# Performance work log

Hardware: AMD Instinct MI355X
Metric: run time of the kernel (lower is better)

## Reference

```python
import jax, jax.numpy as jnp
import numpy as np

N_HEAD, D_HEAD, D_MODEL = 8, 64, 512
QLEN, MLEN, BSZ = 1024, 1024, 4
KLEN = QLEN + MLEN
SCALE = 1.0 / (D_HEAD ** 0.5)
LN_EPS = 1e-5


def _rel_shift(x):
    # x: [qlen, rlen, bsz, n_head]
    q, rl, b, n = x.shape
    zero_pad = jnp.zeros((q, 1, b, n), x.dtype)
    x_padded = jnp.concatenate([zero_pad, x], axis=1).reshape(rl + 1, q, b, n)
    return x_padded[1:].reshape(q, rl, b, n)


def _layer_norm(x, g, b):
    mu = jnp.mean(x, axis=-1, keepdims=True)
    var = jnp.var(x, axis=-1, keepdims=True)
    return (x - mu) * jax.lax.rsqrt(var + LN_EPS) * g + b


def setup_inputs() -> dict:
    key = jax.random.key(0)
    ks = jax.random.split(key, 10)
    s = 0.02
    return {
        "w": jax.random.normal(ks[0], (QLEN, BSZ, D_MODEL), jnp.float32),
        "r": jax.random.normal(ks[1], (KLEN, 1, D_MODEL), jnp.float32),
        "r_w_bias": jax.random.normal(ks[2], (N_HEAD, D_HEAD), jnp.float32) * s,
        "r_r_bias": jax.random.normal(ks[3], (N_HEAD, D_HEAD), jnp.float32) * s,
        "mems": jax.random.normal(ks[4], (MLEN, BSZ, D_MODEL), jnp.float32),
        "Wq": jax.random.normal(ks[5], (D_MODEL, N_HEAD * D_HEAD), jnp.float32) * s,
        "Wkv": jax.random.normal(ks[6], (D_MODEL, 2 * N_HEAD * D_HEAD), jnp.float32) * s,
        "Wr": jax.random.normal(ks[7], (D_MODEL, N_HEAD * D_HEAD), jnp.float32) * s,
        "Wo": jax.random.normal(ks[8], (N_HEAD * D_HEAD, D_MODEL), jnp.float32) * s,
        "ln_g": jnp.ones((D_MODEL,), jnp.float32),
        "ln_b": jnp.zeros((D_MODEL,), jnp.float32),
        # causal mask: query i can attend keys j <= i + MLEN
        "attn_mask": jnp.arange(KLEN)[None, :] > (jnp.arange(QLEN) + MLEN)[:, None],
    }


def reference(w, r, r_w_bias, r_r_bias, mems, Wq, Wkv, Wr, Wo, ln_g, ln_b, attn_mask):
    qlen, bsz = w.shape[0], w.shape[1]
    cat = jnp.concatenate([mems, w], axis=0)          # [klen, bsz, d_model]
    klen = cat.shape[0]

    r_head_k = (r[:, 0] @ Wr).reshape(-1, N_HEAD, D_HEAD)   # [rlen, n, d]
    kv = cat @ Wkv                                           # [klen, bsz, 2*n*d]
    w_head_k, w_head_v = jnp.split(kv, 2, axis=-1)
    w_head_q = (cat[-qlen:] @ Wq).reshape(qlen, bsz, N_HEAD, D_HEAD)
    w_head_k = w_head_k.reshape(klen, bsz, N_HEAD, D_HEAD)
    w_head_v = w_head_v.reshape(klen, bsz, N_HEAD, D_HEAD)

    AC = jnp.einsum('ibnd,jbnd->ijbn', w_head_q + r_w_bias, w_head_k)
    BD = jnp.einsum('ibnd,jnd->ijbn', w_head_q + r_r_bias, r_head_k)
    BD = _rel_shift(BD)[:, :klen]

    attn_score = (AC + BD) * SCALE                           # [qlen, klen, bsz, n]
    attn_score = jnp.where(attn_mask[:, :, None, None], -jnp.inf, attn_score)
    attn_prob = jax.nn.softmax(attn_score, axis=1)

    attn_vec = jnp.einsum('ijbn,jbnd->ibnd', attn_prob, w_head_v)
    attn_vec = attn_vec.reshape(qlen, bsz, N_HEAD * D_HEAD)
    attn_out = attn_vec @ Wo
    return _layer_norm(w + attn_out, ln_g, ln_b)
```

## Files before the change

kernel.cpp:

```cpp
#include <hip/hip_runtime.h>
#include <hip/hip_bf16.h>
#include <math.h>

#define QLEN 1024
#define MLEN 1024
#define KLEN 2048
#define BSZ 4
#define NH 8
#define DH 64
#define DM 512
#define SCALE 0.125f
#define LN_EPS 1e-5f

#define RK_ROWS 2112
#define DSTR 95

typedef __attribute__((ext_vector_type(8))) short short8;
typedef __attribute__((ext_vector_type(4))) float float4_;

#define GLB(p) ((const __attribute__((address_space(1))) void*)(p))
#define LDSP(p) ((__attribute__((address_space(3))) void*)(p))

__device__ inline ushort to_bf16(float x) {
  __hip_bfloat16 h = __float2bfloat16(x);
  return *reinterpret_cast<ushort*>(&h);
}
__device__ inline float bf16_to_f(ushort u) {
  union { unsigned int i; float f; } v;
  v.i = (unsigned int)u << 16;
  return v.f;
}

__device__ inline float row_max16(float v) {
  int x = __builtin_bit_cast(int, v);
  v = fmaxf(v, __builtin_bit_cast(float, __builtin_amdgcn_update_dpp(x, x, 0xB1, 0xF, 0xF, false)));
  x = __builtin_bit_cast(int, v);
  v = fmaxf(v, __builtin_bit_cast(float, __builtin_amdgcn_update_dpp(x, x, 0x4E, 0xF, 0xF, false)));
  x = __builtin_bit_cast(int, v);
  v = fmaxf(v, __builtin_bit_cast(float, __builtin_amdgcn_update_dpp(x, x, 0x124, 0xF, 0xF, false)));
  x = __builtin_bit_cast(int, v);
  v = fmaxf(v, __builtin_bit_cast(float, __builtin_amdgcn_update_dpp(x, x, 0x128, 0xF, 0xF, false)));
  return v;
}
__device__ inline float row_sum16(float v) {
  int x = __builtin_bit_cast(int, v);
  v += __builtin_bit_cast(float, __builtin_amdgcn_update_dpp(x, x, 0xB1, 0xF, 0xF, false));
  x = __builtin_bit_cast(int, v);
  v += __builtin_bit_cast(float, __builtin_amdgcn_update_dpp(x, x, 0x4E, 0xF, 0xF, false));
  x = __builtin_bit_cast(int, v);
  v += __builtin_bit_cast(float, __builtin_amdgcn_update_dpp(x, x, 0x124, 0xF, 0xF, false));
  x = __builtin_bit_cast(int, v);
  v += __builtin_bit_cast(float, __builtin_amdgcn_update_dpp(x, x, 0x128, 0xF, 0xF, false));
  return v;
}

__global__ __launch_bounds__(256) void wtrans_all(
    const float* __restrict__ Wq, const float* __restrict__ Wkv,
    const float* __restrict__ Wr, const float* __restrict__ Wo,
    ushort* __restrict__ WqT, ushort* __restrict__ WkvT,
    ushort* __restrict__ WrT, ushort* __restrict__ WoT) {
  __shared__ ushort tile[32][33];
  const int z = blockIdx.z;
  const float* W;
  ushort* WT;
  int N;
  if (z == 0)      { W = Wq;  WT = WqT;  N = DM; }
  else if (z == 1) { W = Wkv; WT = WkvT; N = 2 * DM; }
  else if (z == 2) { W = Wr;  WT = WrT;  N = DM; }
  else             { W = Wo;  WT = WoT;  N = DM; }
  const int k0 = blockIdx.x * 32, n0 = blockIdx.y * 32;
  if (n0 >= N) return;
  const int tid = threadIdx.x;
#pragma unroll
  for (int it = 0; it < 4; ++it) {
    int idx = tid + it * 256;
    int r = idx >> 5, c = idx & 31;
    tile[r][c] = to_bf16(W[(size_t)(k0 + r) * N + n0 + c]);
  }
  __syncthreads();
#pragma unroll
  for (int it = 0; it < 4; ++it) {
    int idx = tid + it * 256;
    int r = idx >> 5, c = idx & 31;
    WT[(size_t)(n0 + r) * DM + k0 + c] = tile[c][r];
  }
}

__global__ __launch_bounds__(256) void proj_all(
    const float* __restrict__ w, const float* __restrict__ mems,
    const float* __restrict__ r,
    const ushort* __restrict__ WqT, const ushort* __restrict__ WkvT,
    const ushort* __restrict__ WrT,
    const float* __restrict__ bias0, const float* __restrict__ bias1,
    ushort* __restrict__ qw, ushort* __restrict__ qr,
    ushort* __restrict__ k2, ushort* __restrict__ v2,
    ushort* __restrict__ rk2) {
  __shared__ ushort As[128 * 32];
  __shared__ ushort Bs[128 * 32];
  const int tid = threadIdx.x;
  int mode, bx, by;
  {
    int id = blockIdx.x;
    if (id < 128)      { mode = 0; bx = id >> 2;         by = id & 3; }
    else if (id < 640) { mode = 1; bx = (id - 128) >> 3; by = (id - 128) & 7; }
    else               { mode = 2; bx = (id - 640) >> 2; by = (id - 640) & 3; }
  }
  const int m0 = bx * 128, n0 = by * 128;
  const int wv = tid >> 6, lane = tid & 63;
  const int wm = wv >> 1, wn = wv & 1;
  const int l16 = lane & 15, quad = lane >> 4;

  const int arow = tid >> 1;
  const int acol = (tid & 1) * 16;
  const float* asrc;
  {
    int m = m0 + arow;
    if (mode == 2) asrc = r + (size_t)m * DM;
    else asrc = (m < QLEN * BSZ) ? w + (size_t)m * DM
                                 : mems + (size_t)(m - QLEN * BSZ) * DM;
    asrc += acol;
  }
  const ushort* BT = (mode == 0) ? WqT : (mode == 1) ? WkvT : WrT;
  const ushort* bsrc = BT + (size_t)(n0 + arow) * DM + acol;

  float4_ acc[4][4];
#pragma unroll
  for (int a = 0; a < 4; ++a)
#pragma unroll
    for (int b = 0; b < 4; ++b) acc[a][b] = float4_{0.f, 0.f, 0.f, 0.f};

  for (int k0 = 0; k0 < DM; k0 += 32) {
    float4 a0 = *reinterpret_cast<const float4*>(asrc + k0);
    float4 a1 = *reinterpret_cast<const float4*>(asrc + k0 + 4);
    float4 a2 = *reinterpret_cast<const float4*>(asrc + k0 + 8);
    float4 a3 = *reinterpret_cast<const float4*>(asrc + k0 + 12);
    ushort4 u0, u1, u2, u3;
    u0.x = to_bf16(a0.x); u0.y = to_bf16(a0.y); u0.z = to_bf16(a0.z); u0.w = to_bf16(a0.w);
    u1.x = to_bf16(a1.x); u1.y = to_bf16(a1.y); u1.z = to_bf16(a1.z); u1.w = to_bf16(a1.w);
    u2.x = to_bf16(a2.x); u2.y = to_bf16(a2.y); u2.z = to_bf16(a2.z); u2.w = to_bf16(a2.w);
    u3.x = to_bf16(a3.x); u3.y = to_bf16(a3.y); u3.z = to_bf16(a3.z); u3.w = to_bf16(a3.w);
    *reinterpret_cast<ushort4*>(&As[arow * 32 + acol]) = u0;
    *reinterpret_cast<ushort4*>(&As[arow * 32 + acol + 4]) = u1;
    *reinterpret_cast<ushort4*>(&As[arow * 32 + acol + 8]) = u2;
    *reinterpret_cast<ushort4*>(&As[arow * 32 + acol + 12]) = u3;
    *reinterpret_cast<uint4*>(&Bs[arow * 32 + acol]) =
        *reinterpret_cast<const uint4*>(bsrc + k0);
    *reinterpret_cast<uint4*>(&Bs[arow * 32 + acol + 8]) =
        *reinterpret_cast<const uint4*>(bsrc + k0 + 8);
    __syncthreads();
    short8 af[4], bf[4];
#pragma unroll
    for (int f = 0; f < 4; ++f) {
      af[f] = *reinterpret_cast<const short8*>(&As[(wm * 64 + f * 16 + l16) * 32 + quad * 8]);
      bf[f] = *reinterpret_cast<const short8*>(&Bs[(wn * 64 + f * 16 + l16) * 32 + quad * 8]);
    }
#pragma unroll
    for (int fm = 0; fm < 4; ++fm)
#pragma unroll
      for (int fn = 0; fn < 4; ++fn)
        acc[fm][fn] = __builtin_amdgcn_mfma_f32_16x16x32_bf16(bf[fn], af[fm], acc[fm][fn], 0, 0, 0);
    __syncthreads();
  }

#pragma unroll
  for (int fm = 0; fm < 4; ++fm) {
#pragma unroll
    for (int fn = 0; fn < 4; ++fn) {
      const int mm = m0 + wm * 64 + fm * 16 + l16;
      const int nnb = n0 + wn * 64 + fn * 16 + quad * 4;
      const float4_ a = acc[fm][fn];
      if (mode == 0) {
        float4 b0v = *reinterpret_cast<const float4*>(bias0 + nnb);
        float4 b1v = *reinterpret_cast<const float4*>(bias1 + nnb);
        int i = mm >> 2, b = mm & 3;
        int hd = nnb >> 6, d0 = nnb & 63;
        size_t idx = (((size_t)(b * NH + hd)) * QLEN + i) * DH + d0;
        ushort4 o0, o1;
        o0.x = to_bf16(a[0] + b0v.x); o0.y = to_bf16(a[1] + b0v.y);
        o0.z = to_bf16(a[2] + b0v.z); o0.w = to_bf16(a[3] + b0v.w);
        o1.x = to_bf16(a[0] + b1v.x); o1.y = to_bf16(a[1] + b1v.y);
        o1.z = to_bf16(a[2] + b1v.z); o1.w = to_bf16(a[3] + b1v.w);
        *reinterpret_cast<ushort4*>(qw + idx) = o0;
        *reinterpret_cast<ushort4*>(qr + idx) = o1;
      } else if (mode == 1) {
        int pos = mm >> 2, b = mm & 3;
        int jb = pos >> 5, jj = pos & 31;
        if (nnb < DM) {
          int hd = nnb >> 6, d = nnb & 63;
          int bn = b * NH + hd;
          int tile = ((jj >> 4) << 1) | (d >> 5);
          int lane2 = (((d >> 3) & 3) << 4) | (jj & 15);
          ushort4 o;
          o.x = to_bf16(a[0]); o.y = to_bf16(a[1]);
          o.z = to_bf16(a[2]); o.w = to_bf16(a[3]);
          *reinterpret_cast<ushort4*>(
              k2 + ((((size_t)bn * 64 + jb) * 4 + tile) * 64 + lane2) * 8 + (d & 7)) = o;
        } else {
          int nn2 = nnb - DM;
          int hd = nn2 >> 6, d = nn2 & 63;
          int bn = b * NH + hd;
          int tile = d >> 4;
          size_t base = ((((size_t)bn * 64 + jb) * 4 + tile) * 64 +
                         ((jj >> 3) << 4)) * 8 + (jj & 7);
#pragma unroll
          for (int reg = 0; reg < 4; ++reg)
            v2[base + (size_t)((d & 15) + reg) * 8] = to_bf16(a[reg]);
        }
      } else {
        int t = mm;
        int hd = nnb >> 6, d = nnb & 63;
        ushort4 o;
        o.x = to_bf16(a[0]); o.y = to_bf16(a[1]);
        o.z = to_bf16(a[2]); o.w = to_bf16(a[3]);
        *reinterpret_cast<ushort4*>(
            rk2 + ((size_t)hd * RK_ROWS + t) * DH + d) = o;
      }
    }
  }
}

__device__ inline uint4 combine8(uint4 u0, uint4 u1, float s0, float s1) {
  union U { uint4 v; ushort u[8]; };
  U a, b, o;
  a.v = u0; b.v = u1;
#pragma unroll
  for (int e = 0; e < 8; ++e)
    o.u[e] = to_bf16(bf16_to_f(a.u[e]) * s0 + bf16_to_f(b.u[e]) * s1);
  return o.v;
}

__global__ __launch_bounds__(256) void mfma_out(
    const ushort* __restrict__ O0, const ushort* __restrict__ O1,
    const float* __restrict__ ml, const ushort* __restrict__ BT,
    float* __restrict__ Y) {
  __shared__ ushort As[128 * 32];
  __shared__ ushort Bs[128 * 32];
  const int tid = threadIdx.x;
  const int m0 = blockIdx.x * 128, n0 = blockIdx.y * 128;
  const int wv = tid >> 6, lane = tid & 63;
  const int wm = wv >> 1, wn = wv & 1;
  const int l16 = lane & 15, quad = lane >> 4;
  const int arow = tid >> 1;
  const int acol = (tid & 1) * 16;
  const int row = m0 + arow;
  const ushort* bsrc = BT + (size_t)(n0 + arow) * DM + acol;
  const float2* mlp = (const float2*)ml;

  float4_ acc[4][4];
#pragma unroll
  for (int a = 0; a < 4; ++a)
#pragma unroll
    for (int b = 0; b < 4; ++b) acc[a][b] = float4_{0.f, 0.f, 0.f, 0.f};

  for (int k0 = 0; k0 < DM; k0 += 32) {
    const int col0 = k0 + acol;
    const int h = col0 >> 6;
    float2 a = mlp[(size_t)row * NH + h];
    float2 c = mlp[(size_t)(QLEN * BSZ + row) * NH + h];
    float M = fmaxf(a.x, c.x);
    float e0 = __builtin_amdgcn_exp2f(a.x - M);
    float e1 = __builtin_amdgcn_exp2f(c.x - M);
    float inv = 1.f / (a.y * e0 + c.y * e1);
    float s0 = e0 * inv, s1 = e1 * inv;
    size_t ob = (size_t)row * DM + col0;
    uint4 u0a = *reinterpret_cast<const uint4*>(O0 + ob);
    uint4 u0b = *reinterpret_cast<const uint4*>(O0 + ob + 8);
    uint4 u1a = *reinterpret_cast<const uint4*>(O1 + ob);
    uint4 u1b = *reinterpret_cast<const uint4*>(O1 + ob + 8);
    *reinterpret_cast<uint4*>(&As[arow * 32 + acol]) = combine8(u0a, u1a, s0, s1);
    *reinterpret_cast<uint4*>(&As[arow * 32 + acol + 8]) = combine8(u0b, u1b, s0, s1);
    *reinterpret_cast<uint4*>(&Bs[arow * 32 + acol]) = *reinterpret_cast<const uint4*>(bsrc + k0);
    *reinterpret_cast<uint4*>(&Bs[arow * 32 + acol + 8]) = *reinterpret_cast<const uint4*>(bsrc + k0 + 8);
    __syncthreads();
    short8 af[4], bf[4];
#pragma unroll
    for (int f = 0; f < 4; ++f) {
      af[f] = *reinterpret_cast<const short8*>(&As[(wm * 64 + f * 16 + l16) * 32 + quad * 8]);
      bf[f] = *reinterpret_cast<const short8*>(&Bs[(wn * 64 + f * 16 + l16) * 32 + quad * 8]);
    }
#pragma unroll
    for (int fm = 0; fm < 4; ++fm)
#pragma unroll
      for (int fn = 0; fn < 4; ++fn)
        acc[fm][fn] = __builtin_amdgcn_mfma_f32_16x16x32_bf16(bf[fn], af[fm], acc[fm][fn], 0, 0, 0);
    __syncthreads();
  }
#pragma unroll
  for (int fm = 0; fm < 4; ++fm)
#pragma unroll
    for (int fn = 0; fn < 4; ++fn) {
      int mm = m0 + wm * 64 + fm * 16 + l16;
      int nnb = n0 + wn * 64 + fn * 16 + quad * 4;
      float4 o;
      o.x = acc[fm][fn][0]; o.y = acc[fm][fn][1];
      o.z = acc[fm][fn][2]; o.w = acc[fm][fn][3];
      *reinterpret_cast<float4*>(Y + (size_t)mm * DM + nnb) = o;
    }
}

__global__ __launch_bounds__(256) void ln_fuse(
    const float* __restrict__ y, const float* __restrict__ wres,
    const float* __restrict__ g, const float* __restrict__ bb,
    float* __restrict__ out) {
  const int row = blockIdx.x * 4 + (threadIdx.x >> 6);
  const int lane = threadIdx.x & 63;
  const float* yr = y + (size_t)row * DM + lane * 4;
  const float* wr = wres + (size_t)row * DM + lane * 4;
  float4 x0 = *(const float4*)yr;
  float4 x1 = *(const float4*)(yr + 256);
  float4 w0 = *(const float4*)wr;
  float4 w1 = *(const float4*)(wr + 256);
  x0.x += w0.x; x0.y += w0.y; x0.z += w0.z; x0.w += w0.w;
  x1.x += w1.x; x1.y += w1.y; x1.z += w1.z; x1.w += w1.w;
  float s = x0.x + x0.y + x0.z + x0.w + x1.x + x1.y + x1.z + x1.w;
  float ss = x0.x * x0.x + x0.y * x0.y + x0.z * x0.z + x0.w * x0.w +
             x1.x * x1.x + x1.y * x1.y + x1.z * x1.z + x1.w * x1.w;
#pragma unroll
  for (int off = 1; off <= 32; off <<= 1) {
    s += __shfl_xor(s, off, 64);
    ss += __shfl_xor(ss, off, 64);
  }
  float mu = s * (1.f / DM);
  float var = ss * (1.f / DM) - mu * mu;
  float rstd = rsqrtf(var + LN_EPS);
  float4 g0 = *(const float4*)(g + lane * 4);
  float4 g1 = *(const float4*)(g + lane * 4 + 256);
  float4 b0 = *(const float4*)(bb + lane * 4);
  float4 b1 = *(const float4*)(bb + lane * 4 + 256);
  float4 o0, o1;
  o0.x = (x0.x - mu) * rstd * g0.x + b0.x;
  o0.y = (x0.y - mu) * rstd * g0.y + b0.y;
  o0.z = (x0.z - mu) * rstd * g0.z + b0.z;
  o0.w = (x0.w - mu) * rstd * g0.w + b0.w;
  o1.x = (x1.x - mu) * rstd * g1.x + b1.x;
  o1.y = (x1.y - mu) * rstd * g1.y + b1.y;
  o1.z = (x1.z - mu) * rstd * g1.z + b1.z;
  o1.w = (x1.w - mu) * rstd * g1.w + b1.w;
  float* orow = out + (size_t)row * DM + lane * 4;
  *reinterpret_cast<float4*>(orow) = o0;
  *reinterpret_cast<float4*>(orow + 256) = o1;
}

__global__ __launch_bounds__(256, 2) void attn_mfma(
    const ushort* __restrict__ qw, const ushort* __restrict__ qr,
    const ushort* __restrict__ k2, const ushort* __restrict__ v2,
    const ushort* __restrict__ rk2, ushort* __restrict__ Opart,
    float* __restrict__ ml) {
  const int i0b = (gridDim.x - 1 - blockIdx.x) * 64;
  const int n = blockIdx.y;
  const int b = blockIdx.z >> 1, seg = blockIdx.z & 1;
  const int bn = b * NH + n;
  const int tid = threadIdx.x;
  const int wv = tid >> 6, lane = tid & 63;
  const int l16 = lane & 15, quad = lane >> 4;
  const int i0w = i0b + wv * 16;

  __shared__ ushort stage[2][16 * 512];
  __shared__ float Dlds[4][16 * DSTR];
  __shared__ ushort Plds[4][1024];
  float* __restrict__ Dw = Dlds[wv];
  ushort* __restrict__ Pw = Plds[wv];

  const ushort* __restrict__ k2b = k2 + (size_t)bn * (64 * 4 * 512);
  const ushort* __restrict__ v2b = v2 + (size_t)bn * (64 * 4 * 512);
  const ushort* __restrict__ rk2n = rk2 + (size_t)n * RK_ROWS * DH;

  const int nIterTot = i0b / 64 + 17;
  const int nHalf = nIterTot >> 1;
  const int c0 = seg ? nHalf : 0;
  const int c1 = seg ? nIterTot : nHalf;

  short8 aqw0, aqw1, aqr0, aqr1;
  {
    const ushort* qwp = qw + (((size_t)bn * QLEN) + i0w + l16) * DH + quad * 8;
    const ushort* qrp = qr + (((size_t)bn * QLEN) + i0w + l16) * DH + quad * 8;
    aqw0 = *(const short8*)(qwp);
    aqw1 = *(const short8*)(qwp + 32);
    aqr0 = *(const short8*)(qrp);
    aqr1 = *(const short8*)(qrp + 32);
  }

  auto issue_dma = [&](int jb, int buf) {
#pragma unroll
    for (int s = 0; s < 4; ++s) {
      const int m = wv + s * 4;
      const int mk = m & 7;
      const ushort* base = (m < 8) ? k2b : v2b;
      const ushort* g = base +
          ((size_t)(jb * 2 + (mk >> 2)) * 4 + (mk & 3)) * 512 + lane * 8;
      __builtin_amdgcn_global_load_lds(GLB(g), LDSP(&stage[buf][m * 512]), 16, 0, 0);
    }
  };

  float4_ O[4];
#pragma unroll
  for (int t = 0; t < 4; ++t) O[t] = float4_{0.f, 0.f, 0.f, 0.f};
  float mrow[4] = {-INFINITY, -INFINITY, -INFINITY, -INFINITY};
  float lpart[4] = {0.f, 0.f, 0.f, 0.f};
  const float SL2E = SCALE * 1.44269504088896f;

  short8 rbA0[5], rbA1[5], rbN0[5], rbN1[5];

  issue_dma(c0, 0);
  {
    const int tb0 = c0 * 64 - i0b + 1008 - 16 * wv + l16;
#pragma unroll
    for (int tt = 0; tt < 5; ++tt) {
      const ushort* rrow = rk2n + (size_t)(tb0 + tt * 16) * DH;
      rbA0[tt] = *(const short8*)(rrow + quad * 8);
      rbA1[tt] = *(const short8*)(rrow + (4 + quad) * 8);
    }
  }
  issue_dma(c0 + 1, 1);

  for (int k = c0; k < c1; ++k) {
    __builtin_amdgcn_s_waitcnt(0x0F74);
    __builtin_amdgcn_sched_barrier(0);
    __builtin_amdgcn_s_barrier();
    __builtin_amdgcn_sched_barrier(0);
    const ushort* sb = stage[(k - c0) & 1];
    const int j0 = k * 64;

    __builtin_amdgcn_s_setprio(1);
    float4_ ac[4];
#pragma unroll
    for (int h = 0; h < 4; ++h) {
      const ushort* kb = sb + (((h >> 1) * 4 + (h & 1) * 2) * 512) + lane * 8;
      short8 b0 = *(const short8*)(kb);
      short8 b1 = *(const short8*)(kb + 512);
      float4_ c = {0.f, 0.f, 0.f, 0.f};
      c = __builtin_amdgcn_mfma_f32_16x16x32_bf16(aqw0, b0, c, 0, 0, 0);
      c = __builtin_amdgcn_mfma_f32_16x16x32_bf16(aqw1, b1, c, 0, 0, 0);
      ac[h] = c;
    }
#pragma unroll
    for (int tt = 0; tt < 5; ++tt) {
      float4_ d = {0.f, 0.f, 0.f, 0.f};
      d = __builtin_amdgcn_mfma_f32_16x16x32_bf16(aqr0, rbA0[tt], d, 0, 0, 0);
      d = __builtin_amdgcn_mfma_f32_16x16x32_bf16(aqr1, rbA1[tt], d, 0, 0, 0);
#pragma unroll
      for (int rg = 0; rg < 4; ++rg) {
        int row = quad * 4 + rg;
        Dw[row * DSTR + tt * 16 + l16 + row] = d[rg];
      }
    }
    __builtin_amdgcn_s_setprio(0);

    {
      int kn = k + 1; if (kn > c1 - 1) kn = c1 - 1;
      const int tbN = kn * 64 - i0b + 1008 - 16 * wv + l16;
#pragma unroll
      for (int tt = 0; tt < 5; ++tt) {
        const ushort* rrow = rk2n + (size_t)(tbN + tt * 16) * DH;
        rbN0[tt] = *(const short8*)(rrow + quad * 8);
        rbN1[tt] = *(const short8*)(rrow + (4 + quad) * 8);
      }
    }

    float s4[4][4];
#pragma unroll
    for (int hh = 0; hh < 4; ++hh)
#pragma unroll
      for (int rg = 0; rg < 4; ++rg) {
        int row = quad * 4 + rg;
        int jloc = hh * 16 + l16;
        float bd = Dw[row * DSTR + jloc + 15];
        float sv = (ac[hh][rg] + bd) * SL2E;
        s4[hh][rg] = (j0 + jloc > i0w + row + MLEN) ? -INFINITY : sv;
      }
#pragma unroll
    for (int rg = 0; rg < 4; ++rg) {
      float mx = row_max16(fmaxf(fmaxf(s4[0][rg], s4[1][rg]),
                                 fmaxf(s4[2][rg], s4[3][rg])));
      float mn = fmaxf(mrow[rg], mx);
      float alpha = __builtin_amdgcn_exp2f(mrow[rg] - mn);
      float p0 = __builtin_amdgcn_exp2f(s4[0][rg] - mn);
      float p1 = __builtin_amdgcn_exp2f(s4[1][rg] - mn);
      float p2 = __builtin_amdgcn_exp2f(s4[2][rg] - mn);
      float p3 = __builtin_amdgcn_exp2f(s4[3][rg] - mn);
      lpart[rg] = lpart[rg] * alpha + (p0 + p1 + p2 + p3);
      mrow[rg] = mn;
#pragma unroll
      for (int t = 0; t < 4; ++t) O[t][rg] *= alpha;
      int row = quad * 4 + rg;
      int pbase = (l16 >> 3) * 128 + row * 8 + (l16 & 7);
      Pw[pbase]       = to_bf16(p0);
      Pw[pbase + 256] = to_bf16(p1);
      Pw[pbase + 512] = to_bf16(p2);
      Pw[pbase + 768] = to_bf16(p3);
    }
    short8 pf0 = *(const short8*)(Pw + lane * 8);
    short8 pf1 = *(const short8*)(Pw + 512 + lane * 8);
    __builtin_amdgcn_s_setprio(1);
#pragma unroll
    for (int t = 0; t < 4; ++t) {
      short8 vf0 = *(const short8*)(sb + (8 + t) * 512 + lane * 8);
      short8 vf1 = *(const short8*)(sb + (12 + t) * 512 + lane * 8);
      O[t] = __builtin_amdgcn_mfma_f32_16x16x32_bf16(pf0, vf0, O[t], 0, 0, 0);
      O[t] = __builtin_amdgcn_mfma_f32_16x16x32_bf16(pf1, vf1, O[t], 0, 0, 0);
    }
    __builtin_amdgcn_s_setprio(0);

    __builtin_amdgcn_sched_barrier(0);
    __builtin_amdgcn_s_barrier();
    __builtin_amdgcn_sched_barrier(0);
    int jn = k + 2;
    if (jn > c1 - 1) jn = c1 - 1;
    issue_dma(jn, (k - c0) & 1);
#pragma unroll
    for (int tt = 0; tt < 5; ++tt) { rbA0[tt] = rbN0[tt]; rbA1[tt] = rbN1[tt]; }
  }

  float lsum[4];
#pragma unroll
  for (int rg = 0; rg < 4; ++rg) lsum[rg] = row_sum16(lpart[rg]);
  ushort* op = Opart + (size_t)seg * QLEN * BSZ * DM;
  float2* mlp = (float2*)ml;
#pragma unroll
  for (int rg = 0; rg < 4; ++rg) {
    int row = quad * 4 + rg;
    if (l16 == 0) {
      mlp[((size_t)seg * QLEN * BSZ + (size_t)(i0w + row) * BSZ + b) * NH + n] =
          float2{mrow[rg], lsum[rg]};
    }
#pragma unroll
    for (int t = 0; t < 4; ++t) {
      op[((size_t)(i0w + row) * BSZ + b) * DM + n * DH + t * 16 + l16] =
          to_bf16(O[t][rg]);
    }
  }
}

extern "C" void kernel_launch(void* const* d_in, const int* in_sizes, int n_in,
                              void* d_out, int out_size, void* d_ws, size_t ws_size,
                              hipStream_t stream) {
  const float* w    = (const float*)d_in[0];
  const float* r    = (const float*)d_in[1];
  const float* rwb  = (const float*)d_in[2];
  const float* rrb  = (const float*)d_in[3];
  const float* mems = (const float*)d_in[4];
  const float* Wq   = (const float*)d_in[5];
  const float* Wkv  = (const float*)d_in[6];
  const float* Wr   = (const float*)d_in[7];
  const float* Wo   = (const float*)d_in[8];
  const float* ln_g = (const float*)d_in[9];
  const float* ln_b = (const float*)d_in[10];
  float* out = (float*)d_out;

  char* p = (char*)d_ws;
  auto alloc = [&](size_t bytes) {
    char* q = p;
    p += (bytes + 255) & ~(size_t)255;
    return q;
  };
  ushort* WqT   = (ushort*)alloc((size_t)DM * DM * 2);
  ushort* WkvT  = (ushort*)alloc((size_t)2 * DM * DM * 2);
  ushort* WrT   = (ushort*)alloc((size_t)DM * DM * 2);
  ushort* WoT   = (ushort*)alloc((size_t)DM * DM * 2);
  ushort* qw    = (ushort*)alloc((size_t)BSZ * NH * QLEN * DH * 2);
  ushort* qr    = (ushort*)alloc((size_t)BSZ * NH * QLEN * DH * 2);
  ushort* k2    = (ushort*)alloc((size_t)BSZ * NH * 64 * 4 * 512 * 2);
  ushort* v2    = (ushort*)alloc((size_t)BSZ * NH * 64 * 4 * 512 * 2);
  ushort* rk2   = (ushort*)alloc((size_t)NH * RK_ROWS * DH * 2);
  ushort* Opart = (ushort*)alloc((size_t)2 * QLEN * BSZ * DM * 2);
  float*  ml    = (float*)alloc((size_t)2 * QLEN * BSZ * NH * 2 * 4);
  float* y = (float*)k2;

  wtrans_all<<<dim3(16, 32, 4), dim3(256), 0, stream>>>(
      Wq, Wkv, Wr, Wo, WqT, WkvT, WrT, WoT);
  proj_all<<<dim3(704), dim3(256), 0, stream>>>(
      w, mems, r, WqT, WkvT, WrT, rwb, rrb, qw, qr, k2, v2, rk2);
  attn_mfma<<<dim3(QLEN / 64, NH, BSZ * 2), dim3(256), 0, stream>>>(
      qw, qr, k2, v2, rk2, Opart, ml);
  mfma_out<<<dim3(32, 4), dim3(256), 0, stream>>>(
      Opart, Opart + (size_t)QLEN * BSZ * DM, ml, WoT, y);
  ln_fuse<<<dim3(QLEN * BSZ / 4), dim3(256), 0, stream>>>(y, w, ln_g, ln_b, out);
}
```

Measured before the change: 262.3 us.

## Give each attention wave 32 query rows and read K/V straight from global

The attention kernel now gives each wave two 16-row query groups, so each block covers 128 rows. K/V fragments are reused across both groups, and the rel-shift BD tile is shared across them through a reorganised LDS buffer. The double-buffered global_load_lds staging, barriers and priority hints are removed. K/V fragments are now loaded directly from global memory, and the V layout written by the projection kernel changes to match. The aim is to halve K/V/R traffic per query row and drop barrier overhead, at the cost of exposing global-load latency, raising register pressure and launching half as many blocks.

```diff
diff --git a/kernel.cpp b/kernel.cpp
--- a/kernel.cpp
+++ b/kernel.cpp
@@ -12,14 +12,11 @@
 #define SCALE 0.125f
 #define LN_EPS 1e-5f
 
-#define RK_ROWS 2112
-#define DSTR 95
+#define RK_ROWS 2176
+#define D2STR 36
 
 typedef __attribute__((ext_vector_type(8))) short short8;
 typedef __attribute__((ext_vector_type(4))) float float4_;
-
-#define GLB(p) ((const __attribute__((address_space(1))) void*)(p))
-#define LDSP(p) ((__attribute__((address_space(3))) void*)(p))
 
 __device__ inline ushort to_bf16(float x) {
   __hip_bfloat16 h = __float2bfloat16(x);
@@ -184,8 +181,8 @@
         *reinterpret_cast<ushort4*>(qr + idx) = o1;
       } else if (mode == 1) {
         int pos = mm >> 2, b = mm & 3;
-        int jb = pos >> 5, jj = pos & 31;
         if (nnb < DM) {
+          int jb = pos >> 5, jj = pos & 31;
           int hd = nnb >> 6, d = nnb & 63;
           int bn = b * NH + hd;
           int tile = ((jj >> 4) << 1) | (d >> 5);
@@ -197,14 +194,16 @@
               k2 + ((((size_t)bn * 64 + jb) * 4 + tile) * 64 + lane2) * 8 + (d & 7)) = o;
         } else {
           int nn2 = nnb - DM;
-          int hd = nn2 >> 6, d = nn2 & 63;
+          int hd = nn2 >> 6, dbase = nn2 & 63;
           int bn = b * NH + hd;
-          int tile = d >> 4;
-          size_t base = ((((size_t)bn * 64 + jb) * 4 + tile) * 64 +
-                         ((jj >> 3) << 4)) * 8 + (jj & 7);
+          int jb64 = pos >> 6, j64 = pos & 63;
+          int s_g = (j64 & 15) * 4 + (j64 >> 4);
+          int half = s_g >> 5, s_ = s_g & 31;
+          size_t flat = (((size_t)bn * 32 + jb64) * 8 + (dbase >> 4) * 2 + half) * 512
+                      + (size_t)((s_ >> 3) * 16 + (dbase & 15)) * 8 + (s_ & 7);
 #pragma unroll
           for (int reg = 0; reg < 4; ++reg)
-            v2[base + (size_t)((d & 15) + reg) * 8] = to_bf16(a[reg]);
+            v2[flat + (size_t)reg * 8] = to_bf16(a[reg]);
         }
       } else {
         int t = mm;
@@ -346,187 +345,160 @@
     const ushort* __restrict__ k2, const ushort* __restrict__ v2,
     const ushort* __restrict__ rk2, ushort* __restrict__ Opart,
     float* __restrict__ ml) {
-  const int i0b = (gridDim.x - 1 - blockIdx.x) * 64;
+  const int i0b = (gridDim.x - 1 - blockIdx.x) * 128;
   const int n = blockIdx.y;
   const int b = blockIdx.z >> 1, seg = blockIdx.z & 1;
   const int bn = b * NH + n;
   const int tid = threadIdx.x;
   const int wv = tid >> 6, lane = tid & 63;
   const int l16 = lane & 15, quad = lane >> 4;
-  const int i0w = i0b + wv * 16;
-
-  __shared__ ushort stage[2][16 * 512];
-  __shared__ float Dlds[4][16 * DSTR];
-  __shared__ ushort Plds[4][1024];
-  float* __restrict__ Dw = Dlds[wv];
-  ushort* __restrict__ Pw = Plds[wv];
+  const int i0w = i0b + wv * 32;
+
+  __shared__ float D2all[4][96 * D2STR];
+  __shared__ ushort Pall[4][1024];
+  float* __restrict__ Dw = D2all[wv];
+  ushort* __restrict__ Pw = Pall[wv];
 
   const ushort* __restrict__ k2b = k2 + (size_t)bn * (64 * 4 * 512);
-  const ushort* __restrict__ v2b = v2 + (size_t)bn * (64 * 4 * 512);
+  const ushort* __restrict__ v2b = v2 + (size_t)bn * (32 * 8 * 512);
   const ushort* __restrict__ rk2n = rk2 + (size_t)n * RK_ROWS * DH;
 
-  const int nIterTot = i0b / 64 + 17;
+  const int nIterTot = i0b / 64 + 18;
   const int nHalf = nIterTot >> 1;
   const int c0 = seg ? nHalf : 0;
   const int c1 = seg ? nIterTot : nHalf;
 
-  short8 aqw0, aqw1, aqr0, aqr1;
-  {
-    const ushort* qwp = qw + (((size_t)bn * QLEN) + i0w + l16) * DH + quad * 8;
-    const ushort* qrp = qr + (((size_t)bn * QLEN) + i0w + l16) * DH + quad * 8;
-    aqw0 = *(const short8*)(qwp);
-    aqw1 = *(const short8*)(qwp + 32);
-    aqr0 = *(const short8*)(qrp);
-    aqr1 = *(const short8*)(qrp + 32);
-  }
-
-  auto issue_dma = [&](int jb, int buf) {
-#pragma unroll
-    for (int s = 0; s < 4; ++s) {
-      const int m = wv + s * 4;
-      const int mk = m & 7;
-      const ushort* base = (m < 8) ? k2b : v2b;
-      const ushort* g = base +
-          ((size_t)(jb * 2 + (mk >> 2)) * 4 + (mk & 3)) * 512 + lane * 8;
-      __builtin_amdgcn_global_load_lds(GLB(g), LDSP(&stage[buf][m * 512]), 16, 0, 0);
-    }
-  };
-
-  float4_ O[4];
-#pragma unroll
-  for (int t = 0; t < 4; ++t) O[t] = float4_{0.f, 0.f, 0.f, 0.f};
-  float mrow[4] = {-INFINITY, -INFINITY, -INFINITY, -INFINITY};
-  float lpart[4] = {0.f, 0.f, 0.f, 0.f};
+  short8 aqw[2][2], aqr[2][2];
+#pragma unroll
+  for (int g = 0; g < 2; ++g) {
+    const ushort* qwp = qw + (((size_t)bn * QLEN) + i0w + g * 16 + l16) * DH + quad * 8;
+    const ushort* qrp = qr + (((size_t)bn * QLEN) + i0w + g * 16 + l16) * DH + quad * 8;
+    aqw[g][0] = *(const short8*)(qwp);
+    aqw[g][1] = *(const short8*)(qwp + 32);
+    aqr[g][0] = *(const short8*)(qrp);
+    aqr[g][1] = *(const short8*)(qrp + 32);
+  }
+
+  float4_ O[2][4];
+  float mrow[2][4], lpart[2][4];
+#pragma unroll
+  for (int g = 0; g < 2; ++g)
+#pragma unroll
+    for (int t = 0; t < 4; ++t) {
+      O[g][t] = float4_{0.f, 0.f, 0.f, 0.f};
+      mrow[g][t] = -INFINITY;
+      lpart[g][t] = 0.f;
+    }
   const float SL2E = SCALE * 1.44269504088896f;
 
-  short8 rbA0[5], rbA1[5], rbN0[5], rbN1[5];
-
-  issue_dma(c0, 0);
-  {
-    const int tb0 = c0 * 64 - i0b + 1008 - 16 * wv + l16;
-#pragma unroll
-    for (int tt = 0; tt < 5; ++tt) {
-      const ushort* rrow = rk2n + (size_t)(tb0 + tt * 16) * DH;
-      rbA0[tt] = *(const short8*)(rrow + quad * 8);
-      rbA1[tt] = *(const short8*)(rrow + (4 + quad) * 8);
-    }
-  }
-  issue_dma(c0 + 1, 1);
-
   for (int k = c0; k < c1; ++k) {
-    __builtin_amdgcn_s_waitcnt(0x0F74);
-    __builtin_amdgcn_sched_barrier(0);
-    __builtin_amdgcn_s_barrier();
-    __builtin_amdgcn_sched_barrier(0);
-    const ushort* sb = stage[(k - c0) & 1];
     const int j0 = k * 64;
 
-    __builtin_amdgcn_s_setprio(1);
-    float4_ ac[4];
+    float4_ ac[2][4];
 #pragma unroll
     for (int h = 0; h < 4; ++h) {
-      const ushort* kb = sb + (((h >> 1) * 4 + (h & 1) * 2) * 512) + lane * 8;
+      const ushort* kb = k2b +
+          ((size_t)(k * 2 + (h >> 1)) * 4 + (h & 1) * 2) * 512 + lane * 8;
       short8 b0 = *(const short8*)(kb);
       short8 b1 = *(const short8*)(kb + 512);
-      float4_ c = {0.f, 0.f, 0.f, 0.f};
-      c = __builtin_amdgcn_mfma_f32_16x16x32_bf16(aqw0, b0, c, 0, 0, 0);
-      c = __builtin_amdgcn_mfma_f32_16x16x32_bf16(aqw1, b1, c, 0, 0, 0);
-      ac[h] = c;
-    }
-#pragma unroll
-    for (int tt = 0; tt < 5; ++tt) {
-      float4_ d = {0.f, 0.f, 0.f, 0.f};
-      d = __builtin_amdgcn_mfma_f32_16x16x32_bf16(aqr0, rbA0[tt], d, 0, 0, 0);
-      d = __builtin_amdgcn_mfma_f32_16x16x32_bf16(aqr1, rbA1[tt], d, 0, 0, 0);
+#pragma unroll
+      for (int g = 0; g < 2; ++g) {
+        float4_ c = {0.f, 0.f, 0.f, 0.f};
+        c = __builtin_amdgcn_mfma_f32_16x16x32_bf16(aqw[g][0], b0, c, 0, 0, 0);
+        c = __builtin_amdgcn_mfma_f32_16x16x32_bf16(aqw[g][1], b1, c, 0, 0, 0);
+        ac[g][h] = c;
+      }
+    }
+
+    const int rb = j0 - i0w + 992;
+#pragma unroll
+    for (int tt = 0; tt < 6; ++tt) {
+      const ushort* rrow = rk2n + (size_t)(rb + tt * 16 + l16) * DH;
+      short8 r0 = *(const short8*)(rrow + quad * 8);
+      short8 r1 = *(const short8*)(rrow + 32 + quad * 8);
+      float* dst = Dw + (tt * 16 + l16) * D2STR + quad * 4;
+      if (tt < 5) {
+        float4_ d = {0.f, 0.f, 0.f, 0.f};
+        d = __builtin_amdgcn_mfma_f32_16x16x32_bf16(aqr[1][0], r0, d, 0, 0, 0);
+        d = __builtin_amdgcn_mfma_f32_16x16x32_bf16(aqr[1][1], r1, d, 0, 0, 0);
+        *reinterpret_cast<float4_*>(dst + 16) = d;
+      }
+      if (tt > 0) {
+        float4_ d = {0.f, 0.f, 0.f, 0.f};
+        d = __builtin_amdgcn_mfma_f32_16x16x32_bf16(aqr[0][0], r0, d, 0, 0, 0);
+        d = __builtin_amdgcn_mfma_f32_16x16x32_bf16(aqr[0][1], r1, d, 0, 0, 0);
+        *reinterpret_cast<float4_*>(dst) = d;
+      }
+    }
+
+    short8 pf[2][2];
+#pragma unroll
+    for (int g = 0; g < 2; ++g) {
+      float s4[4][4];
+#pragma unroll
+      for (int hh = 0; hh < 4; ++hh)
+#pragma unroll
+        for (int rg = 0; rg < 4; ++rg) {
+          int wrow = g * 16 + quad * 4 + rg;
+          float bd = Dw[(hh * 16 + l16 + 31 - wrow) * D2STR + wrow];
+          float sv = (ac[g][hh][rg] + bd) * SL2E;
+          s4[hh][rg] = (j0 + hh * 16 + l16 > i0w + wrow + MLEN) ? -INFINITY : sv;
+        }
 #pragma unroll
       for (int rg = 0; rg < 4; ++rg) {
-        int row = quad * 4 + rg;
-        Dw[row * DSTR + tt * 16 + l16 + row] = d[rg];
-      }
-    }
-    __builtin_amdgcn_s_setprio(0);
-
-    {
-      int kn = k + 1; if (kn > c1 - 1) kn = c1 - 1;
-      const int tbN = kn * 64 - i0b + 1008 - 16 * wv + l16;
-#pragma unroll
-      for (int tt = 0; tt < 5; ++tt) {
-        const ushort* rrow = rk2n + (size_t)(tbN + tt * 16) * DH;
-        rbN0[tt] = *(const short8*)(rrow + quad * 8);
-        rbN1[tt] = *(const short8*)(rrow + (4 + quad) * 8);
-      }
-    }
-
-    float s4[4][4];
-#pragma unroll
-    for (int hh = 0; hh < 4; ++hh)
-#pragma unroll
-      for (int rg = 0; rg < 4; ++rg) {
-        int row = quad * 4 + rg;
-        int jloc = hh * 16 + l16;
-        float bd = Dw[row * DSTR + jloc + 15];
-        float sv = (ac[hh][rg] + bd) * SL2E;
-        s4[hh][rg] = (j0 + jloc > i0w + row + MLEN) ? -INFINITY : sv;
-      }
-#pragma unroll
-    for (int rg = 0; rg < 4; ++rg) {
-      float mx = row_max16(fmaxf(fmaxf(s4[0][rg], s4[1][rg]),
-                                 fmaxf(s4[2][rg], s4[3][rg])));
-      float mn = fmaxf(mrow[rg], mx);
-      float alpha = __builtin_amdgcn_exp2f(mrow[rg] - mn);
-      float p0 = __builtin_amdgcn_exp2f(s4[0][rg] - mn);
-      float p1 = __builtin_amdgcn_exp2f(s4[1][rg] - mn);
-      float p2 = __builtin_amdgcn_exp2f(s4[2][rg] - mn);
-      float p3 = __builtin_amdgcn_exp2f(s4[3][rg] - mn);
-      lpart[rg] = lpart[rg] * alpha + (p0 + p1 + p2 + p3);
-      mrow[rg] = mn;
-#pragma unroll
-      for (int t = 0; t < 4; ++t) O[t][rg] *= alpha;
-      int row = quad * 4 + rg;
-      int pbase = (l16 >> 3) * 128 + row * 8 + (l16 & 7);
-      Pw[pbase]       = to_bf16(p0);
-      Pw[pbase + 256] = to_bf16(p1);
-      Pw[pbase + 512] = to_bf16(p2);
-      Pw[pbase + 768] = to_bf16(p3);
-    }
-    short8 pf0 = *(const short8*)(Pw + lane * 8);
-    short8 pf1 = *(const short8*)(Pw + 512 + lane * 8);
-    __builtin_amdgcn_s_setprio(1);
+        float mx = row_max16(fmaxf(fmaxf(s4[0][rg], s4[1][rg]),
+                                   fmaxf(s4[2][rg], s4[3][rg])));
+        float mn = fmaxf(mrow[g][rg], mx);
+        float alpha = __builtin_amdgcn_exp2f(mrow[g][rg] - mn);
+        float p0 = __builtin_amdgcn_exp2f(s4[0][rg] - mn);
+        float p1 = __builtin_amdgcn_exp2f(s4[1][rg] - mn);
+        float p2 = __builtin_amdgcn_exp2f(s4[2][rg] - mn);
+        float p3 = __builtin_amdgcn_exp2f(s4[3][rg] - mn);
+        lpart[g][rg] = lpart[g][rg] * alpha + (p0 + p1 + p2 + p3);
+        mrow[g][rg] = mn;
+#pragma unroll
+        for (int t = 0; t < 4; ++t) O[g][t][rg] *= alpha;
+        unsigned int u0 = (unsigned int)to_bf16(p0) | ((unsigned int)to_bf16(p1) << 16);
+        unsigned int u1 = (unsigned int)to_bf16(p2) | ((unsigned int)to_bf16(p3) << 16);
+        int flat = (l16 >> 1) * 128 + (quad * 4 + rg) * 8 + (l16 & 1) * 4;
+        *reinterpret_cast<uint2*>(Pw + flat) = make_uint2(u0, u1);
+      }
+      pf[g][0] = *(const short8*)(Pw + lane * 8);
+      pf[g][1] = *(const short8*)(Pw + 512 + lane * 8);
+    }
+
 #pragma unroll
     for (int t = 0; t < 4; ++t) {
-      short8 vf0 = *(const short8*)(sb + (8 + t) * 512 + lane * 8);
-      short8 vf1 = *(const short8*)(sb + (12 + t) * 512 + lane * 8);
-      O[t] = __builtin_amdgcn_mfma_f32_16x16x32_bf16(pf0, vf0, O[t], 0, 0, 0);
-      O[t] = __builtin_amdgcn_mfma_f32_16x16x32_bf16(pf1, vf1, O[t], 0, 0, 0);
-    }
-    __builtin_amdgcn_s_setprio(0);
-
-    __builtin_amdgcn_sched_barrier(0);
-    __builtin_amdgcn_s_barrier();
-    __builtin_amdgcn_sched_barrier(0);
-    int jn = k + 2;
-    if (jn > c1 - 1) jn = c1 - 1;
-    issue_dma(jn, (k - c0) & 1);
-#pragma unroll
-    for (int tt = 0; tt < 5; ++tt) { rbA0[tt] = rbN0[tt]; rbA1[tt] = rbN1[tt]; }
-  }
-
-  float lsum[4];
-#pragma unroll
-  for (int rg = 0; rg < 4; ++rg) lsum[rg] = row_sum16(lpart[rg]);
+      const ushort* vb = v2b + ((size_t)k * 8 + t * 2) * 512 + lane * 8;
+      short8 vf0 = *(const short8*)(vb);
+      short8 vf1 = *(const short8*)(vb + 512);
+#pragma unroll
+      for (int g = 0; g < 2; ++g) {
+        O[g][t] = __builtin_amdgcn_mfma_f32_16x16x32_bf16(pf[g][0], vf0, O[g][t], 0, 0, 0);
+        O[g][t] = __builtin_amdgcn_mfma_f32_16x16x32_bf16(pf[g][1], vf1, O[g][t], 0, 0, 0);
+      }
+    }
+  }
+
   ushort* op = Opart + (size_t)seg * QLEN * BSZ * DM;
   float2* mlp = (float2*)ml;
 #pragma unroll
-  for (int rg = 0; rg < 4; ++rg) {
-    int row = quad * 4 + rg;
-    if (l16 == 0) {
-      mlp[((size_t)seg * QLEN * BSZ + (size_t)(i0w + row) * BSZ + b) * NH + n] =
-          float2{mrow[rg], lsum[rg]};
-    }
-#pragma unroll
-    for (int t = 0; t < 4; ++t) {
-      op[((size_t)(i0w + row) * BSZ + b) * DM + n * DH + t * 16 + l16] =
-          to_bf16(O[t][rg]);
+  for (int g = 0; g < 2; ++g) {
+    float lsum[4];
+#pragma unroll
+    for (int rg = 0; rg < 4; ++rg) lsum[rg] = row_sum16(lpart[g][rg]);
+#pragma unroll
+    for (int rg = 0; rg < 4; ++rg) {
+      int row = g * 16 + quad * 4 + rg;
+      if (l16 == 0) {
+        mlp[((size_t)seg * QLEN * BSZ + (size_t)(i0w + row) * BSZ + b) * NH + n] =
+            float2{mrow[g][rg], lsum[rg]};
+      }
+#pragma unroll
+      for (int t = 0; t < 4; ++t) {
+        op[((size_t)(i0w + row) * BSZ + b) * DM + n * DH + t * 16 + l16] =
+            to_bf16(O[g][t][rg]);
+      }
     }
   }
 }
@@ -560,7 +532,7 @@
   ushort* qw    = (ushort*)alloc((size_t)BSZ * NH * QLEN * DH * 2);
   ushort* qr    = (ushort*)alloc((size_t)BSZ * NH * QLEN * DH * 2);
   ushort* k2    = (ushort*)alloc((size_t)BSZ * NH * 64 * 4 * 512 * 2);
-  ushort* v2    = (ushort*)alloc((size_t)BSZ * NH * 64 * 4 * 512 * 2);
+  ushort* v2    = (ushort*)alloc((size_t)BSZ * NH * 32 * 8 * 512 * 2);
   ushort* rk2   = (ushort*)alloc((size_t)NH * RK_ROWS * DH * 2);
   ushort* Opart = (ushort*)alloc((size_t)2 * QLEN * BSZ * DM * 2);
   float*  ml    = (float*)alloc((size_t)2 * QLEN * BSZ * NH * 2 * 4);
@@ -570,7 +542,7 @@
       Wq, Wkv, Wr, Wo, WqT, WkvT, WrT, WoT);
   proj_all<<<dim3(704), dim3(256), 0, stream>>>(
       w, mems, r, WqT, WkvT, WrT, rwb, rrb, qw, qr, k2, v2, rk2);
-  attn_mfma<<<dim3(QLEN / 64, NH, BSZ * 2), dim3(256), 0, stream>>>(
+  attn_mfma<<<dim3(QLEN / 128, NH, BSZ * 2), dim3(256), 0, stream>>>(
       qw, qr, k2, v2, rk2, Opart, ml);
   mfma_out<<<dim3(32, 4), dim3(256), 0, stream>>>(
       Opart, Opart + (size_t)QLEN * BSZ * DM, ml, WoT, y);
```

Result: no change. 258.8 us (-1.3%).

## Drop LDS K/V staging; load fragments directly from global, bf16 BD tile

Applied to the files above, without the earlier changes.

Removes the double-buffered global_load_lds staging of K/V tiles and the block-level barriers, so each wave reads K, V and relative-key fragments straight from global/L2 inside the loop. The BD relative-shift buffer is stored as bf16 in a transposed per-wave LDS tile, and the P fragment writes are packed and XOR-swizzled. V is re-laid out in 64-row blocks to match the new direct-load pattern. Occupancy is raised to 4 blocks per CU via the smaller LDS footprint. The trade-off is giving up explicit prefetch overlap in favour of latency hiding through occupancy, and slightly lower BD precision from bf16 storage.

```diff
diff --git a/kernel.cpp b/kernel.cpp
--- a/kernel.cpp
+++ b/kernel.cpp
@@ -12,14 +12,11 @@
 #define SCALE 0.125f
 #define LN_EPS 1e-5f
 
-#define RK_ROWS 2112
-#define DSTR 95
+#define RK_ROWS 2176
+#define D2STR 36
 
 typedef __attribute__((ext_vector_type(8))) short short8;
 typedef __attribute__((ext_vector_type(4))) float float4_;
-
-#define GLB(p) ((const __attribute__((address_space(1))) void*)(p))
-#define LDSP(p) ((__attribute__((address_space(3))) void*)(p))
 
 __device__ inline ushort to_bf16(float x) {
   __hip_bfloat16 h = __float2bfloat16(x);
@@ -184,8 +181,8 @@
         *reinterpret_cast<ushort4*>(qr + idx) = o1;
       } else if (mode == 1) {
         int pos = mm >> 2, b = mm & 3;
-        int jb = pos >> 5, jj = pos & 31;
         if (nnb < DM) {
+          int jb = pos >> 5, jj = pos & 31;
           int hd = nnb >> 6, d = nnb & 63;
           int bn = b * NH + hd;
           int tile = ((jj >> 4) << 1) | (d >> 5);
@@ -197,14 +194,16 @@
               k2 + ((((size_t)bn * 64 + jb) * 4 + tile) * 64 + lane2) * 8 + (d & 7)) = o;
         } else {
           int nn2 = nnb - DM;
-          int hd = nn2 >> 6, d = nn2 & 63;
+          int hd = nn2 >> 6, dbase = nn2 & 63;
           int bn = b * NH + hd;
-          int tile = d >> 4;
-          size_t base = ((((size_t)bn * 64 + jb) * 4 + tile) * 64 +
-                         ((jj >> 3) << 4)) * 8 + (jj & 7);
+          int jb64 = pos >> 6, j64 = pos & 63;
+          int s_g = (j64 & 15) * 4 + (j64 >> 4);
+          int half = s_g >> 5, s_ = s_g & 31;
+          size_t flat = (((size_t)bn * 32 + jb64) * 8 + (dbase >> 4) * 2 + half) * 512
+                      + (size_t)((s_ >> 3) * 16 + (dbase & 15)) * 8 + (s_ & 7);
 #pragma unroll
           for (int reg = 0; reg < 4; ++reg)
-            v2[base + (size_t)((d & 15) + reg) * 8] = to_bf16(a[reg]);
+            v2[flat + (size_t)reg * 8] = to_bf16(a[reg]);
         }
       } else {
         int t = mm;
@@ -341,7 +340,7 @@
   *reinterpret_cast<float4*>(orow + 256) = o1;
 }
 
-__global__ __launch_bounds__(256, 2) void attn_mfma(
+__global__ __launch_bounds__(256, 4) void attn_mfma(
     const ushort* __restrict__ qw, const ushort* __restrict__ qr,
     const ushort* __restrict__ k2, const ushort* __restrict__ v2,
     const ushort* __restrict__ rk2, ushort* __restrict__ Opart,
@@ -355,18 +354,17 @@
   const int l16 = lane & 15, quad = lane >> 4;
   const int i0w = i0b + wv * 16;
 
-  __shared__ ushort stage[2][16 * 512];
-  __shared__ float Dlds[4][16 * DSTR];
-  __shared__ ushort Plds[4][1024];
-  float* __restrict__ Dw = Dlds[wv];
-  ushort* __restrict__ Pw = Plds[wv];
+  __shared__ ushort D2all[4][80 * D2STR];
+  __shared__ ushort Pall[4][1024];
+  ushort* __restrict__ Dw = D2all[wv];
+  ushort* __restrict__ Pw = Pall[wv];
 
   const ushort* __restrict__ k2b = k2 + (size_t)bn * (64 * 4 * 512);
-  const ushort* __restrict__ v2b = v2 + (size_t)bn * (64 * 4 * 512);
+  const ushort* __restrict__ v2b = v2 + (size_t)bn * (32 * 8 * 512);
   const ushort* __restrict__ rk2n = rk2 + (size_t)n * RK_ROWS * DH;
 
   const int nIterTot = i0b / 64 + 17;
-  const int nHalf = nIterTot >> 1;
+  const int nHalf = (nIterTot + 1) >> 1;
   const int c0 = seg ? nHalf : 0;
   const int c1 = seg ? nIterTot : nHalf;
 
@@ -380,18 +378,6 @@
     aqr1 = *(const short8*)(qrp + 32);
   }
 
-  auto issue_dma = [&](int jb, int buf) {
-#pragma unroll
-    for (int s = 0; s < 4; ++s) {
-      const int m = wv + s * 4;
-      const int mk = m & 7;
-      const ushort* base = (m < 8) ? k2b : v2b;
-      const ushort* g = base +
-          ((size_t)(jb * 2 + (mk >> 2)) * 4 + (mk & 3)) * 512 + lane * 8;
-      __builtin_amdgcn_global_load_lds(GLB(g), LDSP(&stage[buf][m * 512]), 16, 0, 0);
-    }
-  };
-
   float4_ O[4];
 #pragma unroll
   for (int t = 0; t < 4; ++t) O[t] = float4_{0.f, 0.f, 0.f, 0.f};
@@ -399,33 +385,17 @@
   float lpart[4] = {0.f, 0.f, 0.f, 0.f};
   const float SL2E = SCALE * 1.44269504088896f;
 
-  short8 rbA0[5], rbA1[5], rbN0[5], rbN1[5];
-
-  issue_dma(c0, 0);
-  {
-    const int tb0 = c0 * 64 - i0b + 1008 - 16 * wv + l16;
-#pragma unroll
-    for (int tt = 0; tt < 5; ++tt) {
-      const ushort* rrow = rk2n + (size_t)(tb0 + tt * 16) * DH;
-      rbA0[tt] = *(const short8*)(rrow + quad * 8);
-      rbA1[tt] = *(const short8*)(rrow + (4 + quad) * 8);
-    }
-  }
-  issue_dma(c0 + 1, 1);
+  const int px = l16 >> 1, ppar = l16 & 1;
 
   for (int k = c0; k < c1; ++k) {
-    __builtin_amdgcn_s_waitcnt(0x0F74);
-    __builtin_amdgcn_sched_barrier(0);
-    __builtin_amdgcn_s_barrier();
-    __builtin_amdgcn_sched_barrier(0);
-    const ushort* sb = stage[(k - c0) & 1];
     const int j0 = k * 64;
 
     __builtin_amdgcn_s_setprio(1);
     float4_ ac[4];
 #pragma unroll
     for (int h = 0; h < 4; ++h) {
-      const ushort* kb = sb + (((h >> 1) * 4 + (h & 1) * 2) * 512) + lane * 8;
+      const ushort* kb = k2b +
+          ((size_t)(k * 2 + (h >> 1)) * 4 + (h & 1) * 2) * 512 + lane * 8;
       short8 b0 = *(const short8*)(kb);
       short8 b1 = *(const short8*)(kb + 512);
       float4_ c = {0.f, 0.f, 0.f, 0.f};
@@ -433,40 +403,32 @@
       c = __builtin_amdgcn_mfma_f32_16x16x32_bf16(aqw1, b1, c, 0, 0, 0);
       ac[h] = c;
     }
-#pragma unroll
-    for (int tt = 0; tt < 5; ++tt) {
+
+    const int rbw = j0 - i0w + 992;
+#pragma unroll
+    for (int tt = 1; tt < 6; ++tt) {
+      const ushort* rrow = rk2n + (size_t)(rbw + tt * 16 + l16) * DH;
+      short8 r0 = *(const short8*)(rrow + quad * 8);
+      short8 r1 = *(const short8*)(rrow + 32 + quad * 8);
       float4_ d = {0.f, 0.f, 0.f, 0.f};
-      d = __builtin_amdgcn_mfma_f32_16x16x32_bf16(aqr0, rbA0[tt], d, 0, 0, 0);
-      d = __builtin_amdgcn_mfma_f32_16x16x32_bf16(aqr1, rbA1[tt], d, 0, 0, 0);
+      d = __builtin_amdgcn_mfma_f32_16x16x32_bf16(aqr0, r0, d, 0, 0, 0);
+      d = __builtin_amdgcn_mfma_f32_16x16x32_bf16(aqr1, r1, d, 0, 0, 0);
+      ushort4 du;
+      du.x = to_bf16(d[0]); du.y = to_bf16(d[1]);
+      du.z = to_bf16(d[2]); du.w = to_bf16(d[3]);
+      *reinterpret_cast<ushort4*>(&Dw[(tt * 16 + l16 - 16) * D2STR + quad * 4]) = du;
+    }
+    __builtin_amdgcn_s_setprio(0);
+
+    float s4[4][4];
+#pragma unroll
+    for (int hh = 0; hh < 4; ++hh)
 #pragma unroll
       for (int rg = 0; rg < 4; ++rg) {
-        int row = quad * 4 + rg;
-        Dw[row * DSTR + tt * 16 + l16 + row] = d[rg];
-      }
-    }
-    __builtin_amdgcn_s_setprio(0);
-
-    {
-      int kn = k + 1; if (kn > c1 - 1) kn = c1 - 1;
-      const int tbN = kn * 64 - i0b + 1008 - 16 * wv + l16;
-#pragma unroll
-      for (int tt = 0; tt < 5; ++tt) {
-        const ushort* rrow = rk2n + (size_t)(tbN + tt * 16) * DH;
-        rbN0[tt] = *(const short8*)(rrow + quad * 8);
-        rbN1[tt] = *(const short8*)(rrow + (4 + quad) * 8);
-      }
-    }
-
-    float s4[4][4];
-#pragma unroll
-    for (int hh = 0; hh < 4; ++hh)
-#pragma unroll
-      for (int rg = 0; rg < 4; ++rg) {
-        int row = quad * 4 + rg;
-        int jloc = hh * 16 + l16;
-        float bd = Dw[row * DSTR + jloc + 15];
+        int wrow = quad * 4 + rg;
+        float bd = bf16_to_f(Dw[(hh * 16 + l16 + 15 - wrow) * D2STR + wrow]);
         float sv = (ac[hh][rg] + bd) * SL2E;
-        s4[hh][rg] = (j0 + jloc > i0w + row + MLEN) ? -INFINITY : sv;
+        s4[hh][rg] = (j0 + hh * 16 + l16 > i0w + wrow + MLEN) ? -INFINITY : sv;
       }
 #pragma unroll
     for (int rg = 0; rg < 4; ++rg) {
@@ -482,33 +444,25 @@
       mrow[rg] = mn;
 #pragma unroll
       for (int t = 0; t < 4; ++t) O[t][rg] *= alpha;
+      unsigned int u0 = (unsigned int)to_bf16(p0) | ((unsigned int)to_bf16(p1) << 16);
+      unsigned int u1 = (unsigned int)to_bf16(p2) | ((unsigned int)to_bf16(p3) << 16);
       int row = quad * 4 + rg;
-      int pbase = (l16 >> 3) * 128 + row * 8 + (l16 & 7);
-      Pw[pbase]       = to_bf16(p0);
-      Pw[pbase + 256] = to_bf16(p1);
-      Pw[pbase + 512] = to_bf16(p2);
-      Pw[pbase + 768] = to_bf16(p3);
-    }
-    short8 pf0 = *(const short8*)(Pw + lane * 8);
-    short8 pf1 = *(const short8*)(Pw + 512 + lane * 8);
+      int off = px * 128 + ((row ^ px)) * 8 + ppar * 4;
+      *reinterpret_cast<uint2*>(Pw + off) = make_uint2(u0, u1);
+    }
+    short8 pf0 = *(const short8*)(Pw + quad * 128 + (l16 ^ quad) * 8);
+    short8 pf1 = *(const short8*)(Pw + 512 + quad * 128 + (l16 ^ (quad + 4)) * 8);
+
     __builtin_amdgcn_s_setprio(1);
 #pragma unroll
     for (int t = 0; t < 4; ++t) {
-      short8 vf0 = *(const short8*)(sb + (8 + t) * 512 + lane * 8);
-      short8 vf1 = *(const short8*)(sb + (12 + t) * 512 + lane * 8);
+      const ushort* vb = v2b + ((size_t)k * 8 + t * 2) * 512 + lane * 8;
+      short8 vf0 = *(const short8*)(vb);
+      short8 vf1 = *(const short8*)(vb + 512);
       O[t] = __builtin_amdgcn_mfma_f32_16x16x32_bf16(pf0, vf0, O[t], 0, 0, 0);
       O[t] = __builtin_amdgcn_mfma_f32_16x16x32_bf16(pf1, vf1, O[t], 0, 0, 0);
     }
     __builtin_amdgcn_s_setprio(0);
-
-    __builtin_amdgcn_sched_barrier(0);
-    __builtin_amdgcn_s_barrier();
-    __builtin_amdgcn_sched_barrier(0);
-    int jn = k + 2;
-    if (jn > c1 - 1) jn = c1 - 1;
-    issue_dma(jn, (k - c0) & 1);
-#pragma unroll
-    for (int tt = 0; tt < 5; ++tt) { rbA0[tt] = rbN0[tt]; rbA1[tt] = rbN1[tt]; }
   }
 
   float lsum[4];
@@ -560,7 +514,7 @@
   ushort* qw    = (ushort*)alloc((size_t)BSZ * NH * QLEN * DH * 2);
   ushort* qr    = (ushort*)alloc((size_t)BSZ * NH * QLEN * DH * 2);
   ushort* k2    = (ushort*)alloc((size_t)BSZ * NH * 64 * 4 * 512 * 2);
-  ushort* v2    = (ushort*)alloc((size_t)BSZ * NH * 64 * 4 * 512 * 2);
+  ushort* v2    = (ushort*)alloc((size_t)BSZ * NH * 32 * 8 * 512 * 2);
   ushort* rk2   = (ushort*)alloc((size_t)NH * RK_ROWS * DH * 2);
   ushort* Opart = (ushort*)alloc((size_t)2 * QLEN * BSZ * DM * 2);
   float*  ml    = (float*)alloc((size_t)2 * QLEN * BSZ * NH * 2 * 4);
```

Result: slower. 288.0 us (+9.8%).
